# Kernel optimization log

Measured on AMD Instinct MI355X. Metric: run time of the kernel, lower is better.

The kernel has to match this reference:

```python
import jax, jax.numpy as jnp
import numpy as np

B, T, D, F, C = 16384, 256, 8, 512, 16  # batch, trees, depth, features, classes
L = 2 ** D  # leaves per tree


def setup_inputs() -> dict:
    key = jax.random.key(0)
    k1, k2, k3, k4 = jax.random.split(key, 4)
    x = jax.random.normal(k1, (B, F), dtype=jnp.float32)
    feature_weights = jax.random.normal(k2, (T, D, F), dtype=jnp.float32)
    thresholds = jax.random.normal(k3, (T, D), dtype=jnp.float32)
    responses = jax.random.normal(k4, (T, L, C), dtype=jnp.float32)
    return {"x": x, "feature_weights": feature_weights,
            "thresholds": thresholds, "responses": responses}


def reference(x, feature_weights, thresholds, responses):
    # Hard feature selection per (tree, level): argmax over features.
    fidx = jnp.argmax(feature_weights, axis=-1)            # [T, D] int
    fv = x[:, fidx]                                        # [B, T, D] gather
    bits = (fv > thresholds[None, :, :]).astype(x.dtype)   # [B, T, D]
    # decision = sum_d bit_d * 2^(D-1-d)  (matches decision*2+bit loop)
    powers = (2 ** jnp.arange(D - 1, -1, -1)).astype(x.dtype)  # [D]
    decision = jnp.sum(bits * powers, axis=-1).astype(jnp.int32)  # [B, T]
    # Gather leaf responses per (sample, tree) and average over trees.
    tree_ids = jnp.arange(T)[None, :]                      # [1, T]
    leaf_out = responses[tree_ids, decision]               # [B, T, C]
    out = jnp.mean(leaf_out, axis=1)                       # [B, C]
    return out  # dropout is identity at eval time
```

## Files before the change

### kernel.cpp

```cpp
#include <hip/hip_runtime.h>

constexpr int B = 16384;
constexpr int T = 256;
constexpr int D = 8;
constexpr int F = 512;
constexpr int C = 16;
constexpr int L = 256;

typedef float f32x4 __attribute__((ext_vector_type(4)));

struct FP { int fidx; float thr; };

__device__ __forceinline__ unsigned int bf16_rne(float f) {
    const unsigned int u = __float_as_uint(f);
    return (u + 0x7fffu + ((u >> 16) & 1u)) >> 16;
}

__global__ __launch_bounds__(256) void prep_kernel(
    const float* __restrict__ fw,
    const float* __restrict__ thr,
    const float* __restrict__ resp,
    FP* __restrict__ packed,
    unsigned int* __restrict__ rb)
{
    if (blockIdx.x < 512) {
        const int wave = threadIdx.x >> 6;
        const int lane = threadIdx.x & 63;
        const int row  = blockIdx.x * 4 + wave;
        const float* base = fw + (size_t)row * F;

        float best = -INFINITY;
        int bidx = 0;
#pragma unroll
        for (int k = 0; k < F / 64; ++k) {
            const int idx = lane + k * 64;
            const float v = base[idx];
            if (v > best) { best = v; bidx = idx; }
        }
#pragma unroll
        for (int off = 32; off >= 1; off >>= 1) {
            const float ov = __shfl_xor(best, off);
            const int   oi = __shfl_xor(bidx, off);
            if (ov > best || (ov == best && oi < bidx)) { best = ov; bidx = oi; }
        }
        if (lane == 0) {
            FP p;
            p.fidx = bidx;
            p.thr  = thr[row];
            packed[row] = p;
        }
    } else {
        const int i = (blockIdx.x - 512) * 256 + threadIdx.x;
        const float4* s = reinterpret_cast<const float4*>(resp) + i * 2;
        const float4 a = s[0], b = s[1];
        uint4 o;
        o.x = bf16_rne(a.x) | (bf16_rne(a.y) << 16);
        o.y = bf16_rne(a.z) | (bf16_rne(a.w) << 16);
        o.z = bf16_rne(b.x) | (bf16_rne(b.y) << 16);
        o.w = bf16_rne(b.z) | (bf16_rne(b.w) << 16);
        reinterpret_cast<uint4*>(rb)[i] = o;
    }
}

__global__ __launch_bounds__(256, 4) void forest_kernel(
    const float* __restrict__ x,
    const FP* __restrict__ packed,
    const unsigned short* __restrict__ rb,
    float* __restrict__ out)
{
    __shared__ float xrow[4][F];
    __shared__ int2  tbl[D][T];

    const int b0  = blockIdx.x * 4;
    const int tid = threadIdx.x;

    {
        const float4* xs = reinterpret_cast<const float4*>(x + (size_t)b0 * F);
        float4* xl = reinterpret_cast<float4*>(&xrow[0][0]);
        xl[tid]       = xs[tid];
        xl[tid + 256] = xs[tid + 256];
    }
    {
        const int4* tp = reinterpret_cast<const int4*>(packed + (size_t)tid * D);
        const int4 q0 = tp[0], q1 = tp[1], q2 = tp[2], q3 = tp[3];
        tbl[0][tid] = make_int2(q0.x, q0.y);
        tbl[1][tid] = make_int2(q0.z, q0.w);
        tbl[2][tid] = make_int2(q1.x, q1.y);
        tbl[3][tid] = make_int2(q1.z, q1.w);
        tbl[4][tid] = make_int2(q2.x, q2.y);
        tbl[5][tid] = make_int2(q2.z, q2.w);
        tbl[6][tid] = make_int2(q3.x, q3.y);
        tbl[7][tid] = make_int2(q3.z, q3.w);
    }
    __syncthreads();

    const int w    = tid >> 6;
    const int lane = tid & 63;

    const float* xb = &xrow[w][0];
    unsigned int dec = 0;
#pragma unroll
    for (int d = 0; d < D; ++d) {
        const int4 a = *reinterpret_cast<const int4*>(&tbl[d][4 * lane]);
        const int4 b = *reinterpret_cast<const int4*>(&tbl[d][4 * lane + 2]);
        const unsigned int bit = 128u >> d;
        if (xb[a.x] > __int_as_float(a.y)) dec |= bit;
        if (xb[a.z] > __int_as_float(a.w)) dec |= bit << 8;
        if (xb[b.x] > __int_as_float(b.y)) dec |= bit << 16;
        if (xb[b.z] > __int_as_float(b.w)) dec |= bit << 24;
    }

    const int src  = lane >> 4;
    const int bsel = ((lane >> 2) & 3) * 8;
    int dw[16];
#pragma unroll
    for (int kk = 0; kk < 16; ++kk) dw[kk] = __shfl((int)dec, 4 * kk + src);

    const int lbase = ((lane >> 2) << 12) | ((lane & 3) << 2);

    uint2 r[16];
#pragma unroll
    for (int kk = 0; kk < 16; ++kk) {
        const int dd = (dw[kk] >> bsel) & 255;
        r[kk] = *reinterpret_cast<const uint2*>(rb + (kk << 16) + (dd << 4) + lbase);
    }

    float4 acc = make_float4(0.f, 0.f, 0.f, 0.f);
#pragma unroll
    for (int kk = 0; kk < 16; ++kk) {
        acc.x += __uint_as_float(r[kk].x << 16);
        acc.y += __uint_as_float(r[kk].x & 0xffff0000u);
        acc.z += __uint_as_float(r[kk].y << 16);
        acc.w += __uint_as_float(r[kk].y & 0xffff0000u);
    }

#pragma unroll
    for (int off = 4; off <= 32; off <<= 1) {
        acc.x += __shfl_xor(acc.x, off);
        acc.y += __shfl_xor(acc.y, off);
        acc.z += __shfl_xor(acc.z, off);
        acc.w += __shfl_xor(acc.w, off);
    }

    if (lane < 4) {
        const float sc = 1.0f / T;
        f32x4 o = { acc.x * sc, acc.y * sc, acc.z * sc, acc.w * sc };
        *reinterpret_cast<f32x4*>(out + ((size_t)(b0 + w) << 4) + (lane << 2)) = o;
    }
}

extern "C" void kernel_launch(void* const* d_in, const int* in_sizes, int n_in,
                              void* d_out, int out_size, void* d_ws, size_t ws_size,
                              hipStream_t stream) {
    const float* x         = (const float*)d_in[0];
    const float* fw        = (const float*)d_in[1];
    const float* thr       = (const float*)d_in[2];
    const float* responses = (const float*)d_in[3];
    float* out             = (float*)d_out;

    FP* packed        = (FP*)d_ws;
    unsigned int* rb  = (unsigned int*)((char*)d_ws + (1 << 16));

    prep_kernel<<<1024, 256, 0, stream>>>(fw, thr, responses, packed, rb);
    forest_kernel<<<B / 4, 256, 0, stream>>>(x, packed,
                                             (const unsigned short*)rb, out);
}
```

Baseline: 100.8 us.

## Process two samples per wave and widen leaf loads to 16 bytes

Each block now handles 8 samples instead of 4, so every wave evaluates two samples and reuses the same tree-table LDS reads for both. The leaf-response gather is remapped so each lane loads 8 bf16 classes (uint4) rather than 4, which halves the number of gather instructions per sample. Grid size halves, and the table load cost is spread over more samples. In exchange, register pressure goes up (16 uint4 plus 16 accumulators), the shuffle reduction tree gets longer, and fewer blocks are available to keep CUs busy.

After: 101.1 us. About the same (+0.3%).

```diff
diff --git a/kernel.cpp b/kernel.cpp
--- a/kernel.cpp
+++ b/kernel.cpp
@@ -68,10 +68,10 @@
     const unsigned short* __restrict__ rb,
     float* __restrict__ out)
 {
-    __shared__ float xrow[4][F];
+    __shared__ float xrow[8][F];
     __shared__ int2  tbl[D][T];
 
-    const int b0  = blockIdx.x * 4;
+    const int b0  = blockIdx.x * 8;
     const int tid = threadIdx.x;
 
     {
@@ -79,6 +79,8 @@
         float4* xl = reinterpret_cast<float4*>(&xrow[0][0]);
         xl[tid]       = xs[tid];
         xl[tid + 256] = xs[tid + 256];
+        xl[tid + 512] = xs[tid + 512];
+        xl[tid + 768] = xs[tid + 768];
     }
     {
         const int4* tp = reinterpret_cast<const int4*>(packed + (size_t)tid * D);
@@ -96,56 +98,95 @@
 
     const int w    = tid >> 6;
     const int lane = tid & 63;
-
-    const float* xb = &xrow[w][0];
-    unsigned int dec = 0;
+    const int sA   = b0 + 2 * w;
+    const int sB   = sA + 1;
+
+    const float* xA = &xrow[2 * w][0];
+    const float* xB = &xrow[2 * w + 1][0];
+    unsigned int decA = 0, decB = 0;
 #pragma unroll
     for (int d = 0; d < D; ++d) {
         const int4 a = *reinterpret_cast<const int4*>(&tbl[d][4 * lane]);
         const int4 b = *reinterpret_cast<const int4*>(&tbl[d][4 * lane + 2]);
+        const float t0 = __int_as_float(a.y), t1 = __int_as_float(a.w);
+        const float t2 = __int_as_float(b.y), t3 = __int_as_float(b.w);
         const unsigned int bit = 128u >> d;
-        if (xb[a.x] > __int_as_float(a.y)) dec |= bit;
-        if (xb[a.z] > __int_as_float(a.w)) dec |= bit << 8;
-        if (xb[b.x] > __int_as_float(b.y)) dec |= bit << 16;
-        if (xb[b.z] > __int_as_float(b.w)) dec |= bit << 24;
-    }
-
-    const int src  = lane >> 4;
-    const int bsel = ((lane >> 2) & 3) * 8;
-    int dw[16];
-#pragma unroll
-    for (int kk = 0; kk < 16; ++kk) dw[kk] = __shfl((int)dec, 4 * kk + src);
-
-    const int lbase = ((lane >> 2) << 12) | ((lane & 3) << 2);
-
-    uint2 r[16];
-#pragma unroll
-    for (int kk = 0; kk < 16; ++kk) {
-        const int dd = (dw[kk] >> bsel) & 255;
-        r[kk] = *reinterpret_cast<const uint2*>(rb + (kk << 16) + (dd << 4) + lbase);
-    }
-
-    float4 acc = make_float4(0.f, 0.f, 0.f, 0.f);
-#pragma unroll
-    for (int kk = 0; kk < 16; ++kk) {
-        acc.x += __uint_as_float(r[kk].x << 16);
-        acc.y += __uint_as_float(r[kk].x & 0xffff0000u);
-        acc.z += __uint_as_float(r[kk].y << 16);
-        acc.w += __uint_as_float(r[kk].y & 0xffff0000u);
-    }
-
-#pragma unroll
-    for (int off = 4; off <= 32; off <<= 1) {
-        acc.x += __shfl_xor(acc.x, off);
-        acc.y += __shfl_xor(acc.y, off);
-        acc.z += __shfl_xor(acc.z, off);
-        acc.w += __shfl_xor(acc.w, off);
-    }
-
-    if (lane < 4) {
-        const float sc = 1.0f / T;
-        f32x4 o = { acc.x * sc, acc.y * sc, acc.z * sc, acc.w * sc };
-        *reinterpret_cast<f32x4*>(out + ((size_t)(b0 + w) << 4) + (lane << 2)) = o;
+        if (xA[a.x] > t0) decA |= bit;
+        if (xA[a.z] > t1) decA |= bit << 8;
+        if (xA[b.x] > t2) decA |= bit << 16;
+        if (xA[b.z] > t3) decA |= bit << 24;
+        if (xB[a.x] > t0) decB |= bit;
+        if (xB[a.z] > t1) decB |= bit << 8;
+        if (xB[b.x] > t2) decB |= bit << 16;
+        if (xB[b.z] > t3) decB |= bit << 24;
+    }
+
+    const int slot = lane >> 1;
+    const int h    = lane & 1;
+    const int srcb = slot >> 2;
+    const int bsel = (slot & 3) * 8;
+    int dwA[8], dwB[8];
+#pragma unroll
+    for (int kk = 0; kk < 8; ++kk) {
+        dwA[kk] = __shfl((int)decA, 8 * kk + srcb);
+        dwB[kk] = __shfl((int)decB, 8 * kk + srcb);
+    }
+
+    const int hoff = h << 3;
+    uint4 rA[8], rB[8];
+#pragma unroll
+    for (int kk = 0; kk < 8; ++kk) {
+        const int ddA = (dwA[kk] >> bsel) & 255;
+        const int ddB = (dwB[kk] >> bsel) & 255;
+        const int tb  = ((kk << 5) + slot) << 12;
+        rA[kk] = *reinterpret_cast<const uint4*>(rb + tb + (ddA << 4) + hoff);
+        rB[kk] = *reinterpret_cast<const uint4*>(rb + tb + (ddB << 4) + hoff);
+    }
+
+    float accA[8] = {0, 0, 0, 0, 0, 0, 0, 0};
+    float accB[8] = {0, 0, 0, 0, 0, 0, 0, 0};
+#pragma unroll
+    for (int kk = 0; kk < 8; ++kk) {
+        accA[0] += __uint_as_float(rA[kk].x << 16);
+        accA[1] += __uint_as_float(rA[kk].x & 0xffff0000u);
+        accA[2] += __uint_as_float(rA[kk].y << 16);
+        accA[3] += __uint_as_float(rA[kk].y & 0xffff0000u);
+        accA[4] += __uint_as_float(rA[kk].z << 16);
+        accA[5] += __uint_as_float(rA[kk].z & 0xffff0000u);
+        accA[6] += __uint_as_float(rA[kk].w << 16);
+        accA[7] += __uint_as_float(rA[kk].w & 0xffff0000u);
+        accB[0] += __uint_as_float(rB[kk].x << 16);
+        accB[1] += __uint_as_float(rB[kk].x & 0xffff0000u);
+        accB[2] += __uint_as_float(rB[kk].y << 16);
+        accB[3] += __uint_as_float(rB[kk].y & 0xffff0000u);
+        accB[4] += __uint_as_float(rB[kk].z << 16);
+        accB[5] += __uint_as_float(rB[kk].z & 0xffff0000u);
+        accB[6] += __uint_as_float(rB[kk].w << 16);
+        accB[7] += __uint_as_float(rB[kk].w & 0xffff0000u);
+    }
+
+#pragma unroll
+    for (int off = 2; off <= 32; off <<= 1) {
+#pragma unroll
+        for (int j = 0; j < 8; ++j) {
+            accA[j] += __shfl_xor(accA[j], off);
+            accB[j] += __shfl_xor(accB[j], off);
+        }
+    }
+
+    const float sc = 1.0f / T;
+    if (lane < 2) {
+        f32x4 v0 = { accA[0] * sc, accA[1] * sc, accA[2] * sc, accA[3] * sc };
+        f32x4 v1 = { accA[4] * sc, accA[5] * sc, accA[6] * sc, accA[7] * sc };
+        float* p = out + ((size_t)sA << 4) + (h << 3);
+        *reinterpret_cast<f32x4*>(p)     = v0;
+        *reinterpret_cast<f32x4*>(p + 4) = v1;
+    } else if (lane < 4) {
+        f32x4 v0 = { accB[0] * sc, accB[1] * sc, accB[2] * sc, accB[3] * sc };
+        f32x4 v1 = { accB[4] * sc, accB[5] * sc, accB[6] * sc, accB[7] * sc };
+        float* p = out + ((size_t)sB << 4) + (h << 3);
+        *reinterpret_cast<f32x4*>(p)     = v0;
+        *reinterpret_cast<f32x4*>(p + 4) = v1;
     }
 }
 
@@ -162,6 +203,6 @@
     unsigned int* rb  = (unsigned int*)((char*)d_ws + (1 << 16));
 
     prep_kernel<<<1024, 256, 0, stream>>>(fw, thr, responses, packed, rb);
-    forest_kernel<<<B / 4, 256, 0, stream>>>(x, packed,
+    forest_kernel<<<B / 8, 256, 0, stream>>>(x, packed,
                                              (const unsigned short*)rb, out);
 }
```
